# Optimization experiments

Measured on AMD Instinct MI355X. Metric: run time of the kernel, lower is better.

## Reference

```python
import jax, jax.numpy as jnp
import numpy as np

FS = 16            # fixStride
LAST_RATIO = 0.5
TAUA, TAUB = 10.0, 0.1
TOT_EPOCHS = 100
EPS = 1e-20
SEED = 777


def _safe_norm(diff):
    # ||diff||_2 with subgradient 0 at 0 (matches torch.norm backward at 0)
    sq = jnp.sum(diff * diff, axis=-1)
    d = jnp.sqrt(jnp.where(sq > 0, sq, 1.0))
    return jnp.where(sq > 0, d, 0.0)


def _forward(x, w_score, b_score, att_params, num_graphs, epoch):
    BN, C = x.shape
    B = int(num_graphs)
    N = BN // B
    RES = N - FS + 1                       # rows per graph (unfold1d)
    MAXP = int(np.ceil(N * LAST_RATIO))    # max_pivot_count = ceil(N*last_ratio/init_ratio)

    # --- TopKPool scorer (init_ratio==1.0): permute nodes per graph by desc score
    scores = (x @ w_score + b_score) / jnp.sqrt(jnp.sum(w_score ** 2))
    perm = jnp.argsort(-scores.reshape(B, N), axis=-1, stable=True)      # [B,N]
    xg = jnp.take_along_axis(x.reshape(B, N, C), perm[..., None], axis=1)

    # --- sliding-window edges: row r -> dests r..r+FS-1, src node r
    dst = jnp.arange(RES)[:, None] + jnp.arange(FS)[None, :]             # [RES,FS]
    x_src = xg[:, :RES, :]                                               # [B,RES,C]
    x_dst = xg[:, dst, :]                                                # [B,RES,FS,C]

    # getSM_ei + scatter_softmax over rows: att = [x_s, x_d] @ att_params
    a1, a2 = att_params[:C], att_params[C:]
    sm = jax.nn.softmax((xg @ a1)[:, :RES, None] + (xg @ a2)[:, dst], axis=-1)  # [B,RES,FS]

    # getDM_ei (sigma=1): gaussian-kernel edge distances
    gk = jnp.exp(-_safe_norm(x_src[:, :, None, :] - x_dst) / 2.0) - EPS  # [B,RES,FS]

    # scatterSort: stable descending sort of gk per row
    order = jnp.argsort(-gk, axis=-1, stable=True)
    gk_sort = jnp.take_along_axis(gk, order, axis=-1)
    sm_sort = jnp.take_along_axis(sm, order, axis=-1)

    # per-rank column logits: scatter-sum of sorted attention over rows of each graph
    logits = jnp.broadcast_to(sm_sort.sum(axis=1)[:, None, :], (B, RES, FS))
    logits = logits.at[:, :, 0].set(-jnp.inf)            # mask rank-0 (self edge)

    # gumbel-softmax with annealed temperature
    tau0 = TAUA * (TAUB / TAUA) ** (float(epoch) / TOT_EPOCHS)
    g = jax.random.gumbel(jax.random.key(SEED), (B, RES, FS), jnp.float32)
    gmb = jax.nn.softmax((g + logits) / tau0, axis=-1)

    # per-row threshold and shifted distances (unsorted layout)
    ths = jnp.sum(gk_sort * gmb, axis=-1, keepdims=True)
    shifted = jax.nn.relu(gk - ths)                      # [B,RES,FS]

    # scatter_min over positions 1..FS-1 (position 0 excluded via index redirect)
    delta = (jnp.argmin(shifted[:, :, 1:], axis=-1) + 1).astype(jnp.int32)  # [B,RES]

    # innerLoopStar: follow skip pointers from row 0, up to MAXP pivots
    def chain(delta_g):
        def step(ptr, _):
            valid = ptr < RES
            piv = jnp.where(valid, ptr, -1)
            nxt = jnp.where(valid, ptr + delta_g[jnp.clip(ptr, 0, RES - 1)], jnp.int32(RES))
            return nxt, piv
        _, pivs = jax.lax.scan(step, jnp.int32(0), None, length=MAXP)
        return pivs

    pivots = jax.vmap(chain)(delta)                      # [B,MAXP], -1 padded
    mask = pivots >= 0
    pooled = jnp.take_along_axis(xg, jnp.clip(pivots, 0, N - 1)[..., None], axis=1)
    pooled = pooled * mask[..., None]                    # [B,MAXP,C]
    return pooled, shifted, pivots


def setup_inputs() -> dict:
    key = jax.random.key(0)
    k0, k1, k2, k3 = jax.random.split(key, 4)
    B, N, C = 128, 512, 64
    return {
        "x": jax.random.normal(k0, (B * N, C), jnp.float32),
        "w_score": jax.random.normal(k1, (C,), jnp.float32),
        "b_score": jax.random.normal(k2, (), jnp.float32),
        "att_params": jax.random.normal(k3, (2 * C,), jnp.float32),
        "num_graphs": B,
        "epoch": 10,
    }


def reference(x, w_score, b_score, att_params, num_graphs, epoch):
    return _forward(x, w_score, b_score, att_params, num_graphs, epoch)
```

## Files before the change

### kernel.cpp

```cpp
#include <hip/hip_runtime.h>
#include <math.h>

#define BB 128
#define NN 512
#define CC 64
#define FS 16
#define RES 497
#define MAXP 256
#define BN (BB*NN)
#define GT (BB*RES*FS)
#define WPB 16
#define NCH 32
#define ROWS (WPB+FS-1)
#define PITCH 66

__device__ __forceinline__ unsigned rotl32(unsigned x, int d){ return (x<<d)|(x>>(32-d)); }

__device__ __forceinline__ void threefry777(unsigned x0, unsigned x1, unsigned &o0, unsigned &o1){
  const unsigned ks0 = 0u, ks1 = 777u;
  const unsigned ks2 = 0x1BD11BDAu ^ ks0 ^ ks1;
  x0 += ks0; x1 += ks1;
  x0+=x1; x1=rotl32(x1,13); x1^=x0;
  x0+=x1; x1=rotl32(x1,15); x1^=x0;
  x0+=x1; x1=rotl32(x1,26); x1^=x0;
  x0+=x1; x1=rotl32(x1, 6); x1^=x0;
  x0+=ks1; x1+=ks2+1u;
  x0+=x1; x1=rotl32(x1,17); x1^=x0;
  x0+=x1; x1=rotl32(x1,29); x1^=x0;
  x0+=x1; x1=rotl32(x1,16); x1^=x0;
  x0+=x1; x1=rotl32(x1,24); x1^=x0;
  x0+=ks2; x1+=ks0+2u;
  x0+=x1; x1=rotl32(x1,13); x1^=x0;
  x0+=x1; x1=rotl32(x1,15); x1^=x0;
  x0+=x1; x1=rotl32(x1,26); x1^=x0;
  x0+=x1; x1=rotl32(x1, 6); x1^=x0;
  x0+=ks0; x1+=ks1+3u;
  x0+=x1; x1=rotl32(x1,17); x1^=x0;
  x0+=x1; x1=rotl32(x1,29); x1^=x0;
  x0+=x1; x1=rotl32(x1,16); x1^=x0;
  x0+=x1; x1=rotl32(x1,24); x1^=x0;
  x0+=ks1; x1+=ks2+4u;
  x0+=x1; x1=rotl32(x1,13); x1^=x0;
  x0+=x1; x1=rotl32(x1,15); x1^=x0;
  x0+=x1; x1=rotl32(x1,26); x1^=x0;
  x0+=x1; x1=rotl32(x1, 6); x1^=x0;
  x0+=ks2; x1+=ks0+5u;
  o0 = x0; o1 = x1;
}

__device__ __forceinline__ float gumbel_at_f32(unsigned p){
  unsigned o0, o1;
  threefry777(0u, p, o0, o1);
  unsigned bits = o0 ^ o1;
  float fl = __uint_as_float((bits >> 9) | 0x3f800000u) - 1.0f;
  float u  = fmaxf(1.17549435e-38f, fl);
  return -logf(-logf(u));
}

__device__ __forceinline__ double wave_push_f64(double v, int dstLane){
  int lo = __double2loint(v), hi = __double2hiint(v);
  int plo = __builtin_amdgcn_ds_permute(dstLane<<2, lo);
  int phi = __builtin_amdgcn_ds_permute(dstLane<<2, hi);
  return __hiloint2double(phi, plo);
}

__global__ __launch_bounds__(NN) void k_scoresort(const float* __restrict__ x,
    const float* __restrict__ w, const float* __restrict__ bsc,
    const float* __restrict__ att, double* __restrict__ s1s,
    double* __restrict__ s2s, int* __restrict__ perm){
  int b = blockIdx.x, t = threadIdx.x;
  __shared__ double ss[NN];
  __shared__ int    si[NN];
  __shared__ double l1[NN], l2[NN];

  double wn=0.0, dw=0.0, d1=0.0, d2=0.0;
  #pragma unroll
  for (int c=0;c<CC;c++){ double wv=(double)w[c]; wn += wv*wv; }
  const float4* xr = (const float4*)(x + (size_t)(b*NN+t)*CC);
  #pragma unroll
  for (int q=0;q<CC/4;q++){
    float4 v = xr[q];
    double xv;
    xv=(double)v.x; dw+=xv*(double)w[4*q+0]; d1+=xv*(double)att[4*q+0]; d2+=xv*(double)att[CC+4*q+0];
    xv=(double)v.y; dw+=xv*(double)w[4*q+1]; d1+=xv*(double)att[4*q+1]; d2+=xv*(double)att[CC+4*q+1];
    xv=(double)v.z; dw+=xv*(double)w[4*q+2]; d1+=xv*(double)att[4*q+2]; d2+=xv*(double)att[CC+4*q+2];
    xv=(double)v.w; dw+=xv*(double)w[4*q+3]; d1+=xv*(double)att[4*q+3]; d2+=xv*(double)att[CC+4*q+3];
  }
  ss[t] = (dw + (double)bsc[0]) / sqrt(wn);
  si[t] = t;
  l1[t] = d1;
  l2[t] = d2;
  __syncthreads();

  for (int k = 2; k <= NN; k <<= 1){
    for (int j = k >> 1; j > 0; j >>= 1){
      int ixj = t ^ j;
      if (ixj > t){
        double s0 = ss[t], s1v = ss[ixj];
        int    i0 = si[t], i1  = si[ixj];
        bool before = (s0 > s1v) || (s0 == s1v && i0 < i1);
        bool up = ((t & k) == 0);
        if (up ? !before : before){
          ss[t] = s1v; ss[ixj] = s0;
          si[t] = i1;  si[ixj] = i0;
        }
      }
      __syncthreads();
    }
  }
  int orig = si[t];
  perm[b*NN + t] = orig;
  s1s[b*NN + t] = l1[orig];
  s2s[b*NN + t] = l2[orig];
}

__global__ __launch_bounds__(256) void k_passA(const float* __restrict__ x,
    const int* __restrict__ perm, const double* __restrict__ s1s,
    const double* __restrict__ s2s, double* __restrict__ gkd,
    unsigned char* __restrict__ rank8, double* __restrict__ partial){
  int b = blockIdx.y, ch = blockIdx.x, tid = threadIdx.x;
  int i0 = ch*WPB;
  int nwin  = min(WPB, RES - i0);
  int nrows = min(ROWS, NN - i0);
  __shared__ float  xs[ROWS*PITCH];
  __shared__ int    pg[ROWS];
  __shared__ double wred[4][FS];

  if (tid < nrows) pg[tid] = perm[b*NN + i0 + tid];
  __syncthreads();
  for (int u = tid; u < nrows*16; u += 256){
    int r = u >> 4, seg = u & 15;
    float4 v = ((const float4*)(x + (size_t)(b*NN + pg[r])*CC))[seg];
    float2* dst = (float2*)&xs[r*PITCH + seg*4];
    dst[0] = make_float2(v.x, v.y);
    dst[1] = make_float2(v.z, v.w);
  }
  __syncthreads();

  int w = tid >> 4, j = tid & 15;
  int lane = tid & 63, gbase = lane & 48, wv = tid >> 6;
  bool act = (w < nwin);
  int i = i0 + w;

  double sq = 0.0;
  const float* rs = &xs[w*PITCH];
  const float* rd = &xs[(w+j)*PITCH];
  #pragma unroll
  for (int c2=0;c2<CC/2;c2++){
    float2 a  = *(const float2*)&rs[2*c2];
    float2 bb = *(const float2*)&rd[2*c2];
    double d0 = (double)a.x - (double)bb.x;
    double d1v= (double)a.y - (double)bb.y;
    sq += d0*d0;
    sq += d1v*d1v;
  }
  double d   = (sq > 0.0) ? sqrt(sq) : 0.0;
  double gkv = exp(-d*0.5) - 1e-20;

  int drow = min(i + j, NN-1);
  double smt = s1s[b*NN + i] + s2s[b*NN + drow];
  double m = smt;
  #pragma unroll
  for (int off=8; off; off>>=1) m = fmax(m, __shfl_xor(m, off, 16));
  double em = exp(smt - m);
  double ssum = em;
  #pragma unroll
  for (int off=8; off; off>>=1) ssum += __shfl_xor(ssum, off, 16);
  double smn = em / ssum;

  int rank = 0;
  #pragma unroll
  for (int k=0;k<16;k++){
    double gkk = __shfl(gkv, gbase + k, 64);
    rank += ((gkk > gkv) || (gkk == gkv && k < j)) ? 1 : 0;
  }

  if (act){
    size_t base = ((size_t)b*RES + i)*FS;
    gkd[base + j]   = gkv;
    rank8[base + j] = (unsigned char)rank;
  }

  double contrib = act ? smn : 0.0;
  double srt = wave_push_f64(contrib, gbase + rank);
  srt += __shfl_xor(srt, 16, 64);
  srt += __shfl_xor(srt, 32, 64);
  if (lane < FS) wred[wv][lane] = srt;
  __syncthreads();
  if (tid < FS){
    partial[((size_t)b*NCH + ch)*FS + tid] =
        wred[0][tid] + wred[1][tid] + wred[2][tid] + wred[3][tid];
  }
}

__global__ void k_colsum(const double* __restrict__ partial, double* __restrict__ colsum){
  int t = blockIdx.x*blockDim.x + threadIdx.x;
  if (t >= BB*FS) return;
  int b = t >> 4, s = t & 15;
  double acc = 0.0;
  #pragma unroll
  for (int ch=0; ch<NCH; ch++) acc += partial[((size_t)b*NCH + ch)*FS + s];
  colsum[t] = acc;
}

__global__ void k_gumbel(const double* __restrict__ gkd, const unsigned char* __restrict__ rank8,
                         const double* __restrict__ colsum, const int* __restrict__ epoch_p,
                         float* __restrict__ shifted_out, int* __restrict__ delta){
  int t = blockIdx.x*blockDim.x + threadIdx.x;
  int win = t >> 4, s = t & 15;
  if (win >= BB*RES) return;
  int lane = threadIdx.x & 63, gbase = lane & 48;
  int b = win / RES;
  size_t base = (size_t)win * FS;
  double tau = 10.0 * pow(0.01, (double)epoch_p[0] / 100.0);

  double z;
  if (s == 0) z = -(double)INFINITY;
  else {
    double g = (double)gumbel_at_f32((unsigned)(base + (unsigned)s));
    z = (g + colsum[b*FS + s]) / tau;
  }
  double m = z;
  #pragma unroll
  for (int off=8; off; off>>=1) m = fmax(m, __shfl_xor(m, off, 16));
  double e = (s == 0) ? 0.0 : exp(z - m);
  double ssum = e;
  #pragma unroll
  for (int off=8; off; off>>=1) ssum += __shfl_xor(ssum, off, 16);
  double gmb = e / ssum;

  double gkv = gkd[base + s];
  int rk = rank8[base + s];
  double gmbr = __shfl(gmb, gbase + rk, 64);
  double ths = gkv * gmbr;
  #pragma unroll
  for (int off=8; off; off>>=1) ths += __shfl_xor(ths, off, 16);

  double shv = fmax(gkv - ths, 0.0);
  shifted_out[base + s] = (float)shv;

  double av = (s == 0) ? (double)INFINITY : shv;
  int ai = s;
  #pragma unroll
  for (int off=8; off; off>>=1){
    double ov = __shfl_xor(av, off, 16);
    int    oi = __shfl_xor(ai, off, 16);
    if (ov < av || (ov == av && oi < ai)){ av = ov; ai = oi; }
  }
  if (s == 0) delta[win] = ai;
}

__global__ __launch_bounds__(256) void k_chain(const int* __restrict__ delta,
                                               float* __restrict__ piv_out,
                                               int* __restrict__ pivi){
  int b = blockIdx.x, tid = threadIdx.x;
  __shared__ int tbl[8][512];
  for (int i = tid; i < 512; i += 256){
    int v;
    if (i < RES){ v = i + delta[b*RES + i]; if (v > RES) v = RES; }
    else v = RES;
    tbl[0][i] = v;
  }
  __syncthreads();
  #pragma unroll
  for (int k=1;k<8;k++){
    int v0 = tbl[k-1][tid];
    int v1 = tbl[k-1][tid+256];
    tbl[k][tid]     = tbl[k-1][v0];
    tbl[k][tid+256] = tbl[k-1][v1];
    __syncthreads();
  }
  int p = 0;
  #pragma unroll
  for (int k=0;k<8;k++) if ((tid>>k)&1) p = tbl[k][p];
  int piv = (p < RES) ? p : -1;
  piv_out[b*MAXP + tid] = (float)piv;
  pivi[b*MAXP + tid]    = piv;
}

__global__ void k_pool(const float* __restrict__ x, const int* __restrict__ perm,
                       const int* __restrict__ pivi, float* __restrict__ pooled){
  int t = blockIdx.x*blockDim.x + threadIdx.x;
  const int total = BB*MAXP*(CC/4);
  if (t >= total) return;
  int c4 = t & 15;
  int bp = t >> 4;
  int piv = pivi[bp];
  float4 v = make_float4(0.f,0.f,0.f,0.f);
  if (piv >= 0){
    int b = bp / MAXP;
    int src = perm[b*NN + piv];
    v = ((const float4*)(x + (size_t)(b*NN + src)*CC))[c4];
  }
  ((float4*)pooled)[t] = v;
}

extern "C" void kernel_launch(void* const* d_in, const int* in_sizes, int n_in,
                              void* d_out, int out_size, void* d_ws, size_t ws_size,
                              hipStream_t stream) {
  (void)in_sizes; (void)n_in; (void)out_size; (void)ws_size;
  const float* x    = (const float*)d_in[0];
  const float* w    = (const float*)d_in[1];
  const float* bsc  = (const float*)d_in[2];
  const float* att  = (const float*)d_in[3];
  const int*   epch = (const int*)d_in[5];

  double* s1s     = (double*)d_ws;
  double* s2s     = s1s + BN;
  double* gkd     = s2s + BN;
  double* partial = gkd + GT;
  double* colsumd = partial + (size_t)BB*NCH*FS;
  int*    perm    = (int*)(colsumd + BB*FS);
  int*    delta   = perm + BN;
  int*    pivi    = delta + BB*RES;
  unsigned char* rank8 = (unsigned char*)(pivi + BB*MAXP);

  float* out_pooled  = (float*)d_out;
  float* out_shifted = out_pooled + BB*MAXP*CC;
  float* out_piv     = out_shifted + (size_t)BB*RES*FS;

  k_scoresort<<<BB, NN, 0, stream>>>(x, w, bsc, att, s1s, s2s, perm);
  k_passA <<<dim3(NCH, BB), 256, 0, stream>>>(x, perm, s1s, s2s, gkd, rank8, partial);
  k_colsum<<<(BB*FS+255)/256, 256, 0, stream>>>(partial, colsumd);
  k_gumbel<<<(BB*RES*16+255)/256, 256, 0, stream>>>(gkd, rank8, colsumd, epch, out_shifted, delta);
  k_chain <<<BB, 256, 0, stream>>>(delta, out_piv, pivi);
  k_pool  <<<(BB*MAXP*(CC/4)+255)/256, 256, 0, stream>>>(x, perm, pivi, out_pooled);
}
```

Baseline: 68.76 us.

## Fuse colsum, gumbel, chain and pool into one per-graph kernel; warp-shuffle bitonic sort

Replaces four tail kernels (colsum, gumbel-softmax, pointer-jumping chain, pooled gather) with one 1024-thread block per graph. The delta table and pivots stay in shared memory instead of round-tripping through global memory, which removes three launches. The bitonic sort in the score kernel now keeps values in registers and uses wave shuffles for strides up to 32, synchronising only for larger strides. In exchange the tail runs only 128 blocks, which may leave the GPU underoccupied in the gumbel phase.

```diff
diff --git a/kernel.cpp b/kernel.cpp
--- a/kernel.cpp
+++ b/kernel.cpp
@@ -86,32 +86,39 @@
     xv=(double)v.z; dw+=xv*(double)w[4*q+2]; d1+=xv*(double)att[4*q+2]; d2+=xv*(double)att[CC+4*q+2];
     xv=(double)v.w; dw+=xv*(double)w[4*q+3]; d1+=xv*(double)att[4*q+3]; d2+=xv*(double)att[CC+4*q+3];
   }
-  ss[t] = (dw + (double)bsc[0]) / sqrt(wn);
-  si[t] = t;
+  double s = (dw + (double)bsc[0]) / sqrt(wn);
+  int idx = t;
   l1[t] = d1;
   l2[t] = d2;
-  __syncthreads();
 
   for (int k = 2; k <= NN; k <<= 1){
-    for (int j = k >> 1; j > 0; j >>= 1){
-      int ixj = t ^ j;
-      if (ixj > t){
-        double s0 = ss[t], s1v = ss[ixj];
-        int    i0 = si[t], i1  = si[ixj];
-        bool before = (s0 > s1v) || (s0 == s1v && i0 < i1);
-        bool up = ((t & k) == 0);
-        if (up ? !before : before){
-          ss[t] = s1v; ss[ixj] = s0;
-          si[t] = i1;  si[ixj] = i0;
-        }
-      }
+    bool up = ((t & k) == 0);
+    for (int j = k >> 1; j >= 64; j >>= 1){
+      ss[t] = s; si[t] = idx;
+      __syncthreads();
+      double os = ss[t ^ j]; int oi = si[t ^ j];
+      bool first = ((t & j) == 0);
+      bool cmp = (s > os) || (s == os && idx < oi);
+      bool keep = (cmp == (first == up));
+      if (!keep){ s = os; idx = oi; }
       __syncthreads();
     }
-  }
-  int orig = si[t];
-  perm[b*NN + t] = orig;
-  s1s[b*NN + t] = l1[orig];
-  s2s[b*NN + t] = l2[orig];
+    #pragma unroll
+    for (int j = 32; j > 0; j >>= 1){
+      if (j <= (k >> 1)){
+        double os = __shfl_xor(s, j, 64);
+        int    oi = __shfl_xor(idx, j, 64);
+        bool first = ((t & j) == 0);
+        bool cmp = (s > os) || (s == os && idx < oi);
+        bool keep = (cmp == (first == up));
+        if (!keep){ s = os; idx = oi; }
+      }
+    }
+  }
+  __syncthreads();
+  perm[b*NN + t] = idx;
+  s1s[b*NN + t] = l1[idx];
+  s2s[b*NN + t] = l2[idx];
 }
 
 __global__ __launch_bounds__(256) void k_passA(const float* __restrict__ x,
@@ -193,106 +200,103 @@
   }
 }
 
-__global__ void k_colsum(const double* __restrict__ partial, double* __restrict__ colsum){
-  int t = blockIdx.x*blockDim.x + threadIdx.x;
-  if (t >= BB*FS) return;
-  int b = t >> 4, s = t & 15;
-  double acc = 0.0;
-  #pragma unroll
-  for (int ch=0; ch<NCH; ch++) acc += partial[((size_t)b*NCH + ch)*FS + s];
-  colsum[t] = acc;
-}
-
-__global__ void k_gumbel(const double* __restrict__ gkd, const unsigned char* __restrict__ rank8,
-                         const double* __restrict__ colsum, const int* __restrict__ epoch_p,
-                         float* __restrict__ shifted_out, int* __restrict__ delta){
-  int t = blockIdx.x*blockDim.x + threadIdx.x;
-  int win = t >> 4, s = t & 15;
-  if (win >= BB*RES) return;
-  int lane = threadIdx.x & 63, gbase = lane & 48;
-  int b = win / RES;
-  size_t base = (size_t)win * FS;
+__global__ __launch_bounds__(1024) void k_tail(const double* __restrict__ gkd,
+    const unsigned char* __restrict__ rank8, const double* __restrict__ partial,
+    const int* __restrict__ epoch_p, const int* __restrict__ perm,
+    const float* __restrict__ x, float* __restrict__ shifted_out,
+    float* __restrict__ piv_out, float* __restrict__ pooled){
+  int b = blockIdx.x, tid = threadIdx.x;
+  __shared__ double pl[NCH*FS];
+  __shared__ double cs[FS];
+  __shared__ int    tbl[8][512];
+  __shared__ int    pivS[MAXP];
+
+  if (tid < NCH*FS) pl[tid] = partial[(size_t)b*NCH*FS + tid];
+  for (int i2 = tid; i2 < 512; i2 += 1024) if (i2 >= RES) tbl[0][i2] = RES;
+  __syncthreads();
+  if (tid < FS){
+    double a = 0.0;
+    #pragma unroll
+    for (int ch=0; ch<NCH; ch++) a += pl[ch*FS + tid];
+    cs[tid] = a;
+  }
+  __syncthreads();
+
   double tau = 10.0 * pow(0.01, (double)epoch_p[0] / 100.0);
-
-  double z;
-  if (s == 0) z = -(double)INFINITY;
-  else {
-    double g = (double)gumbel_at_f32((unsigned)(base + (unsigned)s));
-    z = (g + colsum[b*FS + s]) / tau;
-  }
-  double m = z;
-  #pragma unroll
-  for (int off=8; off; off>>=1) m = fmax(m, __shfl_xor(m, off, 16));
-  double e = (s == 0) ? 0.0 : exp(z - m);
-  double ssum = e;
-  #pragma unroll
-  for (int off=8; off; off>>=1) ssum += __shfl_xor(ssum, off, 16);
-  double gmb = e / ssum;
-
-  double gkv = gkd[base + s];
-  int rk = rank8[base + s];
-  double gmbr = __shfl(gmb, gbase + rk, 64);
-  double ths = gkv * gmbr;
-  #pragma unroll
-  for (int off=8; off; off>>=1) ths += __shfl_xor(ths, off, 16);
-
-  double shv = fmax(gkv - ths, 0.0);
-  shifted_out[base + s] = (float)shv;
-
-  double av = (s == 0) ? (double)INFINITY : shv;
-  int ai = s;
-  #pragma unroll
-  for (int off=8; off; off>>=1){
-    double ov = __shfl_xor(av, off, 16);
-    int    oi = __shfl_xor(ai, off, 16);
-    if (ov < av || (ov == av && oi < ai)){ av = ov; ai = oi; }
-  }
-  if (s == 0) delta[win] = ai;
-}
-
-__global__ __launch_bounds__(256) void k_chain(const int* __restrict__ delta,
-                                               float* __restrict__ piv_out,
-                                               int* __restrict__ pivi){
-  int b = blockIdx.x, tid = threadIdx.x;
-  __shared__ int tbl[8][512];
-  for (int i = tid; i < 512; i += 256){
-    int v;
-    if (i < RES){ v = i + delta[b*RES + i]; if (v > RES) v = RES; }
-    else v = RES;
-    tbl[0][i] = v;
-  }
-  __syncthreads();
+  int lane = tid & 63, gbase = lane & 48;
+  int s = tid & 15;
+
+  #pragma unroll
+  for (int it=0; it<8; it++){
+    int win = it*64 + (tid >> 4);
+    if (win < RES){
+      size_t base = ((size_t)b*RES + win)*FS;
+      double z;
+      if (s == 0) z = -(double)INFINITY;
+      else {
+        double g = (double)gumbel_at_f32((unsigned)(base + (unsigned)s));
+        z = (g + cs[s]) / tau;
+      }
+      double m = z;
+      #pragma unroll
+      for (int off=8; off; off>>=1) m = fmax(m, __shfl_xor(m, off, 16));
+      double e = (s == 0) ? 0.0 : exp(z - m);
+      double ssum = e;
+      #pragma unroll
+      for (int off=8; off; off>>=1) ssum += __shfl_xor(ssum, off, 16);
+      double gmb = e / ssum;
+
+      double gkv = gkd[base + s];
+      int rk = rank8[base + s];
+      double gmbr = __shfl(gmb, gbase + rk, 64);
+      double ths = gkv * gmbr;
+      #pragma unroll
+      for (int off=8; off; off>>=1) ths += __shfl_xor(ths, off, 16);
+
+      double shv = fmax(gkv - ths, 0.0);
+      shifted_out[base + s] = (float)shv;
+
+      double av = (s == 0) ? (double)INFINITY : shv;
+      int ai = s;
+      #pragma unroll
+      for (int off=8; off; off>>=1){
+        double ov = __shfl_xor(av, off, 16);
+        int    oi = __shfl_xor(ai, off, 16);
+        if (ov < av || (ov == av && oi < ai)){ av = ov; ai = oi; }
+      }
+      if (s == 0){
+        int v = win + ai;
+        tbl[0][win] = (v > RES) ? RES : v;
+      }
+    }
+  }
+  __syncthreads();
+
   #pragma unroll
   for (int k=1;k<8;k++){
-    int v0 = tbl[k-1][tid];
-    int v1 = tbl[k-1][tid+256];
-    tbl[k][tid]     = tbl[k-1][v0];
-    tbl[k][tid+256] = tbl[k-1][v1];
+    if (tid < 512){ int v = tbl[k-1][tid]; tbl[k][tid] = tbl[k-1][v]; }
     __syncthreads();
   }
-  int p = 0;
-  #pragma unroll
-  for (int k=0;k<8;k++) if ((tid>>k)&1) p = tbl[k][p];
-  int piv = (p < RES) ? p : -1;
-  piv_out[b*MAXP + tid] = (float)piv;
-  pivi[b*MAXP + tid]    = piv;
-}
-
-__global__ void k_pool(const float* __restrict__ x, const int* __restrict__ perm,
-                       const int* __restrict__ pivi, float* __restrict__ pooled){
-  int t = blockIdx.x*blockDim.x + threadIdx.x;
-  const int total = BB*MAXP*(CC/4);
-  if (t >= total) return;
-  int c4 = t & 15;
-  int bp = t >> 4;
-  int piv = pivi[bp];
-  float4 v = make_float4(0.f,0.f,0.f,0.f);
-  if (piv >= 0){
-    int b = bp / MAXP;
-    int src = perm[b*NN + piv];
-    v = ((const float4*)(x + (size_t)(b*NN + src)*CC))[c4];
-  }
-  ((float4*)pooled)[t] = v;
+  if (tid < MAXP){
+    int p = 0;
+    #pragma unroll
+    for (int k=0;k<8;k++) if ((tid>>k)&1) p = tbl[k][p];
+    int piv = (p < RES) ? p : -1;
+    pivS[tid] = piv;
+    piv_out[b*MAXP + tid] = (float)piv;
+  }
+  __syncthreads();
+
+  for (int u = tid; u < MAXP*16; u += 1024){
+    int bp = u >> 4, seg = u & 15;
+    int piv = pivS[bp];
+    float4 v = make_float4(0.f,0.f,0.f,0.f);
+    if (piv >= 0){
+      int src = perm[b*NN + piv];
+      v = ((const float4*)(x + (size_t)(b*NN + src)*CC))[seg];
+    }
+    ((float4*)pooled)[(size_t)(b*MAXP + bp)*16 + seg] = v;
+  }
 }
 
 extern "C" void kernel_launch(void* const* d_in, const int* in_sizes, int n_in,
@@ -309,11 +313,8 @@
   double* s2s     = s1s + BN;
   double* gkd     = s2s + BN;
   double* partial = gkd + GT;
-  double* colsumd = partial + (size_t)BB*NCH*FS;
-  int*    perm    = (int*)(colsumd + BB*FS);
-  int*    delta   = perm + BN;
-  int*    pivi    = delta + BB*RES;
-  unsigned char* rank8 = (unsigned char*)(pivi + BB*MAXP);
+  int*    perm    = (int*)(partial + (size_t)BB*NCH*FS);
+  unsigned char* rank8 = (unsigned char*)(perm + BN);
 
   float* out_pooled  = (float*)d_out;
   float* out_shifted = out_pooled + BB*MAXP*CC;
@@ -321,8 +322,6 @@
 
   k_scoresort<<<BB, NN, 0, stream>>>(x, w, bsc, att, s1s, s2s, perm);
   k_passA <<<dim3(NCH, BB), 256, 0, stream>>>(x, perm, s1s, s2s, gkd, rank8, partial);
-  k_colsum<<<(BB*FS+255)/256, 256, 0, stream>>>(partial, colsumd);
-  k_gumbel<<<(BB*RES*16+255)/256, 256, 0, stream>>>(gkd, rank8, colsumd, epch, out_shifted, delta);
-  k_chain <<<BB, 256, 0, stream>>>(delta, out_piv, pivi);
-  k_pool  <<<(BB*MAXP*(CC/4)+255)/256, 256, 0, stream>>>(x, perm, pivi, out_pooled);
-}
+  k_tail  <<<BB, 1024, 0, stream>>>(gkd, rank8, partial, epch, perm, x,
+                                    out_shifted, out_piv, out_pooled);
+}
```

New measurement: 66.39 us. 3.4% less time.
